# Optimization experiments

Measured on AMD Instinct MI355X. Metric: run time of the kernel, lower is better.

## Reference

```python
import jax, jax.numpy as jnp
import numpy as np
from jax import lax

B, N, C, RED = 8, 2048, 1024, 4
GN_EPS = 1e-5


def setup_inputs() -> dict:
    key = jax.random.key(0)
    ks = jax.random.split(key, 8)
    s = lambda k, shp, sc: jax.random.normal(k, shp, jnp.float32) * sc
    return dict(
        x=jax.random.normal(ks[0], (B, N, C), jnp.float32),
        qkv_w=s(ks[1], (C, 3 * C), 0.02),
        c1=jnp.float32(0.01 ** 2),
        c2=jnp.float32(0.03 ** 2),
        conv1_w=s(ks[2], (4, 1, 3), 0.3),      # OIH
        gn_g=jnp.ones(4, jnp.float32),
        gn_b=jnp.zeros(4, jnp.float32),
        conv2_w=s(ks[3], (1, 4, 3), 0.3),      # OIH
        conv2_b=jnp.zeros(1, jnp.float32),
        ch_w1=s(ks[4], (C, C // RED), 0.02),
        ch_b1=jnp.zeros(C // RED, jnp.float32),
        ch_w2=s(ks[5], (C // RED, C), 0.02),
        ch_b2=jnp.zeros(C, jnp.float32),
        proj_w=s(ks[6], (C, C), 0.02),
        proj_b=jnp.zeros(C, jnp.float32),
    )


def _conv1d(x, w):  # x:[B,Cin,N], w:[O,I,3], pad=1
    return lax.conv_general_dilated(x, w, (1,), [(1, 1)],
                                    dimension_numbers=('NCH', 'OIH', 'NCH'))


def _ode_func(A, conv1_w, gn_g, gn_b, conv2_w, conv2_b):
    # A: [B,N] -> Conv1d(1,4) -> GroupNorm(2,4) -> ReLU -> Conv1d(4,1)
    h = _conv1d(A[:, None, :], conv1_w)                 # [B,4,N]
    b, _, n = h.shape
    hg = h.reshape(b, 2, 2, n)                          # 2 groups of 2 channels
    mu = hg.mean((2, 3), keepdims=True)
    var = hg.var((2, 3), keepdims=True)
    h = ((hg - mu) * lax.rsqrt(var + GN_EPS)).reshape(b, 4, n)
    h = jax.nn.relu(h * gn_g[None, :, None] + gn_b[None, :, None])
    y = _conv1d(h, conv2_w) + conv2_b[None, :, None]    # [B,1,N]
    return y[:, 0, :]


def reference(x, qkv_w, c1, c2, conv1_w, gn_g, gn_b, conv2_w, conv2_b,
              ch_w1, ch_b1, ch_w2, ch_b2, proj_w, proj_b):
    Bx, Nx, Cx = x.shape
    qkv = (x @ qkv_w).reshape(Bx, Nx, 3, Cx)
    q, k, v = qkv[..., 0, :], qkv[..., 1, :], qkv[..., 2, :]

    # SSIM-style per-token statistics over the channel dim
    mu_q = q.mean(-1, keepdims=True)
    mu_k = k.mean(-1, keepdims=True)
    dq, dk = q - mu_q, k - mu_k
    inv_cm1 = 1.0 / (Cx - 1)
    sigma_qk = (dq * dk).sum(-1, keepdims=True) * inv_cm1
    sigma_q2 = (dq * dq).sum(-1, keepdims=True) * inv_cm1
    sigma_k2 = (dk * dk).sum(-1, keepdims=True) * inv_cm1
    num = (2 * mu_q * mu_k + c1) * (2 * sigma_qk + c2)
    den = (mu_q ** 2 + mu_k ** 2 + c1) * (sigma_q2 + sigma_k2 + c2)
    attn_base = ((num / (den + 1e-7)) ** 2)[..., 0]     # [B,N]

    # explicit-Euler integration over t = linspace(0,1,2) -> one step, dt=1
    steps = 2
    ts = jnp.linspace(0.0, 1.0, steps)
    dts = ts[1:] - ts[:-1]

    def step(A, dt):
        return A + dt * _ode_func(A, conv1_w, gn_g, gn_b, conv2_w, conv2_b), None

    A, _ = lax.scan(step, attn_base, dts)
    final_a = jax.nn.sigmoid(A)                         # [B,N]
    weights = jax.nn.softmax(final_a, axis=1)           # softmax over tokens

    # channel gating from mean token
    m = x.mean(axis=1, keepdims=True)                   # [B,1,C]
    ch_w = jax.nn.sigmoid(jax.nn.relu(m @ ch_w1 + ch_b1) @ ch_w2 + ch_b2)

    out_low = weights[..., None] * v * ch_w             # [B,N,C]
    return out_low @ proj_w + proj_b
```

## Files before the change

### kernel.cpp

```cpp
#include <hip/hip_runtime.h>

typedef __attribute__((ext_vector_type(8))) short short8;
typedef __attribute__((ext_vector_type(4))) short short4v;
typedef __attribute__((ext_vector_type(4))) float floatx4;

__device__ __forceinline__ unsigned short f2bf(float f) {
    unsigned u = __float_as_uint(f);
    u = u + 0x7fffu + ((u >> 16) & 1u);
    return (unsigned short)(u >> 16);
}

__device__ __forceinline__ void gl_lds16(const void* g, void* l) {
    __builtin_amdgcn_global_load_lds((const __attribute__((address_space(1))) void*)g,
                                     (__attribute__((address_space(3))) void*)l, 16, 0, 0);
}

__global__ __launch_bounds__(256) void convmean_kernel(const float* __restrict__ x,
                                                       short* __restrict__ xb,
                                                       float* __restrict__ part) {
    int bid = blockIdx.x;
    int b = bid >> 6, nch = bid & 63;
    int tid = threadIdx.x;
    size_t base = ((size_t)b * 2048 + nch * 32) * 1024;
    float s0 = 0.f, s1 = 0.f, s2 = 0.f, s3 = 0.f;
    int c0 = tid * 4;
    for (int r = 0; r < 32; r++) {
        const float* rp = x + base + (size_t)r * 1024 + c0;
        float4 v = *(const float4*)rp;
        s0 += v.x; s1 += v.y; s2 += v.z; s3 += v.w;
        short4v o;
        o[0] = (short)f2bf(v.x); o[1] = (short)f2bf(v.y);
        o[2] = (short)f2bf(v.z); o[3] = (short)f2bf(v.w);
        *(short4v*)(xb + base + (size_t)r * 1024 + c0) = o;
    }
    float* pp = part + ((size_t)b * 64 + nch) * 1024 + c0;
    float4 ps; ps.x = s0; ps.y = s1; ps.z = s2; ps.w = s3;
    *(float4*)pp = ps;
}

__global__ __launch_bounds__(256) void transpose_conv_kernel(const float* __restrict__ w_qkv,
                                                             short* __restrict__ qkvT,
                                                             const float* __restrict__ w_proj,
                                                             short* __restrict__ projT) {
    __shared__ float t[64][65];
    int bx = blockIdx.x;
    const float* in; short* out; int C; bool is_qkv;
    int c0, r0 = blockIdx.y * 64;
    if (bx < 48) { in = w_qkv; out = qkvT; C = 3072; c0 = bx * 64; is_qkv = true; }
    else         { in = w_proj; out = projT; C = 1024; c0 = (bx - 48) * 64; is_qkv = false; }
    int tid = threadIdx.x;
#pragma unroll
    for (int l = 0; l < 16; l++) {
        int idx = l * 256 + tid;
        int rr = idx >> 6, cc = idx & 63;
        t[rr][cc] = in[(size_t)(r0 + rr) * C + c0 + cc];
    }
    __syncthreads();
#pragma unroll
    for (int l = 0; l < 16; l++) {
        int idx = l * 256 + tid;
        int rr = idx >> 6, cc = idx & 63;
        int ro = c0 + rr;
        int rnew = ro;
        if (is_qkv) {
            if (ro < 1024) rnew = 2 * ro;
            else if (ro < 2048) rnew = 2 * (ro - 1024) + 1;
        }
        out[(size_t)rnew * 1024 + r0 + cc] = (short)f2bf(t[cc][rr]);
    }
}

__global__ __launch_bounds__(256) void ch_kernel(const float* __restrict__ part,
                                                 const float* __restrict__ w1,
                                                 const float* __restrict__ b1,
                                                 const float* __restrict__ w2,
                                                 const float* __restrict__ b2,
                                                 float* __restrict__ ch) {
    int b = blockIdx.x >> 3, cg = blockIdx.x & 7;
    int tid = threadIdx.x;
    __shared__ float mrow[1024];
    __shared__ float hid[256];
    for (int i = tid; i < 1024; i += 256) {
        float s = 0.f;
        for (int j = 0; j < 64; j++) s += part[((size_t)b * 64 + j) * 1024 + i];
        mrow[i] = s * (1.f / 2048.f);
    }
    __syncthreads();
    {
        float s0 = 0.f, s1 = 0.f, s2 = 0.f, s3 = 0.f;
        for (int i = 0; i < 1024; i += 4) {
            s0 += mrow[i] * w1[(size_t)i * 256 + tid];
            s1 += mrow[i + 1] * w1[(size_t)(i + 1) * 256 + tid];
            s2 += mrow[i + 2] * w1[(size_t)(i + 2) * 256 + tid];
            s3 += mrow[i + 3] * w1[(size_t)(i + 3) * 256 + tid];
        }
        hid[tid] = fmaxf((s0 + s1) + (s2 + s3) + b1[tid], 0.f);
    }
    __syncthreads();
    if (tid < 128) {
        int c = cg * 128 + tid;
        float s0 = 0.f, s1 = 0.f, s2 = 0.f, s3 = 0.f;
        for (int j = 0; j < 256; j += 4) {
            s0 += hid[j] * w2[(size_t)j * 1024 + c];
            s1 += hid[j + 1] * w2[(size_t)(j + 1) * 1024 + c];
            s2 += hid[j + 2] * w2[(size_t)(j + 2) * 1024 + c];
            s3 += hid[j + 3] * w2[(size_t)(j + 3) * 1024 + c];
        }
        float s = (s0 + s1) + (s2 + s3) + b2[c];
        ch[(size_t)b * 1024 + c] = 1.f / (1.f + expf(-s));
    }
}


#define KLOOP_BODY(T)                                                                   \
    {                                                                                   \
        const short* As_ = SH + ((T) & 1) * 4096;                                       \
        const short* Bs_ = SH + 8192 + ((T) & 1) * 8192;                                \
        _Pragma("unroll")                                                               \
        for (int jj = 0; jj < 4; jj++)                                                  \
            bfr[jj] = *(const short8*)(Bs_ + (wn * 64 + jj * 16 + ar) * 32 + swq);      \
        _Pragma("unroll")                                                               \
        for (int ii = 0; ii < 4; ii++)                                                  \
            af[ii] = *(const short8*)(As_ + (wm * 64 + ii * 16 + ar) * 32 + swq);       \
        __builtin_amdgcn_s_setprio(1);                                                  \
        _Pragma("unroll")                                                               \
        for (int ii = 0; ii < 4; ii++)                                                  \
            _Pragma("unroll")                                                           \
            for (int jj = 0; jj < 4; jj++)                                              \
                acc[ii][jj] =                                                           \
                    __builtin_amdgcn_mfma_f32_16x16x32_bf16(af[ii], bfr[jj], acc[ii][jj], 0, 0, 0); \
        __builtin_amdgcn_s_setprio(0);                                                  \
    }

__global__ __launch_bounds__(512, 4) void gemm_qkv_kernel(const short* __restrict__ A,
                                                          const short* __restrict__ BT,
                                                          short* __restrict__ vbuf,
                                                          const float* __restrict__ ch,
                                                          float* __restrict__ part2)
{
    __shared__ __align__(16) short SH[2 * 4096 + 2 * 8192];
    const int tid = threadIdx.x;
    const int wave = tid >> 6, lane = tid & 63;
    const int id = blockIdx.x;
    const int xcd = id & 7, j = id >> 3;
    const int bn = j % 12;
    const int bmg = j / 12;
    const int bm = bmg * 8 + xcd;
    const int wm = wave >> 2, wn = wave & 3;
    const int ar = lane & 15, quad = lane >> 4;
    const int swq = (quad ^ ((ar >> 1) & 3)) * 8;

    const int swzk = ((lane & 3) ^ ((lane >> 3) & 3)) * 8;
    const short* Ag = A + (size_t)(bm * 128 + wave * 16 + (lane >> 2)) * 1024 + swzk;
    const short* Bg = BT + (size_t)(bn * 256 + wave * 32 + (lane >> 2)) * 1024 + swzk;
    short* ASw = SH + wave * 512;
    short* BSw = SH + 8192 + wave * 1024;

    floatx4 acc[4][4];
    floatx4 zero = {0.f, 0.f, 0.f, 0.f};
#pragma unroll
    for (int i = 0; i < 4; i++)
#pragma unroll
        for (int jj = 0; jj < 4; jj++) acc[i][jj] = zero;

    auto stage = [&](int t) {
        const int sa = (t & 1) * 4096, sb2 = (t & 1) * 8192, ko = t * 32;
        gl_lds16(Ag + ko, ASw + sa);
        gl_lds16(Bg + ko, BSw + sb2);
        gl_lds16(Bg + (size_t)16 * 1024 + ko, BSw + sb2 + 512);
    };

    short8 af[4], bfr[4];

    stage(0);
    for (int t = 0; t < 31; ++t) {
        stage(t + 1);
        asm volatile("s_waitcnt vmcnt(3)" ::: "memory");
        asm volatile("s_barrier" ::: "memory");
        KLOOP_BODY(t);
        asm volatile("s_barrier" ::: "memory");
    }
    asm volatile("s_waitcnt vmcnt(0)" ::: "memory");
    asm volatile("s_barrier" ::: "memory");
    KLOOP_BODY(31);
    __syncthreads();

    if (bn < 8) {
        float* sb = (float*)SH;
#pragma unroll
        for (int i = 0; i < 4; i++) {
            float st[4][5];
#pragma unroll
            for (int r = 0; r < 4; r++)
#pragma unroll
                for (int f = 0; f < 5; f++) st[r][f] = 0.f;
#pragma unroll
            for (int jj = 0; jj < 4; jj++) {
#pragma unroll
                for (int r = 0; r < 4; r++) {
                    float val = acc[i][jj][r];
                    float other = __shfl_xor(val, 1);
                    float q = (lane & 1) ? other : val;
                    float kv = (lane & 1) ? val : other;
                    st[r][0] += q; st[r][1] += kv;
                    st[r][2] += q * q; st[r][3] += kv * kv; st[r][4] += q * kv;
                }
            }
#pragma unroll
            for (int r = 0; r < 4; r++)
#pragma unroll
                for (int f = 0; f < 5; f++) {
                    float v = st[r][f];
                    v += __shfl_xor(v, 2);
                    v += __shfl_xor(v, 4);
                    v += __shfl_xor(v, 8);
                    st[r][f] = v;
                }
            if ((lane & 15) == 0) {
#pragma unroll
                for (int r = 0; r < 4; r++)
#pragma unroll
                    for (int f = 0; f < 5; f++)
                        sb[(size_t)(wn * 128 + wm * 64 + i * 16 + quad * 4 + r) * 5 + f] = st[r][f];
            }
        }
        __syncthreads();
        if (tid < 128) {
#pragma unroll
            for (int f = 0; f < 5; f++) {
                float s = sb[(size_t)(0 * 128 + tid) * 5 + f] + sb[(size_t)(1 * 128 + tid) * 5 + f] +
                          sb[(size_t)(2 * 128 + tid) * 5 + f] + sb[(size_t)(3 * 128 + tid) * 5 + f];
                part2[(size_t)(bn * 5 + f) * 16384 + bm * 128 + tid] = s;
            }
        }
    } else {
        const int batch = bm >> 4;
        const int vcol0 = bn * 256 - 2048 + wn * 64;
        short* pbuf = SH + wave * 1024;
        float cw[4];
#pragma unroll
        for (int jj = 0; jj < 4; jj++) cw[jj] = ch[(size_t)batch * 1024 + vcol0 + jj * 16 + ar];
#pragma unroll
        for (int i = 0; i < 4; i++) {
#pragma unroll
            for (int jj = 0; jj < 4; jj++)
#pragma unroll
                for (int r = 0; r < 4; r++)
                    pbuf[(quad * 4 + r) * 64 + jj * 16 + ar] = (short)f2bf(acc[i][jj][r] * cw[jj]);
#pragma unroll
            for (int p = 0; p < 2; p++) {
                int idx = p * 512 + lane * 8;
                short8 vv = *(const short8*)(pbuf + idx);
                int grow = bm * 128 + wm * 64 + i * 16 + (idx >> 6);
                int gcol = vcol0 + (idx & 63);
                *(short8*)(vbuf + (size_t)grow * 1024 + gcol) = vv;
            }
        }
    }
}

__global__ __launch_bounds__(256) void finalize_kernel(const float* __restrict__ part2,
                                                       const float* __restrict__ c1p,
                                                       const float* __restrict__ c2p,
                                                       float* __restrict__ attn) {
    int row = blockIdx.x * 256 + threadIdx.x;
    float s[5] = {0.f, 0.f, 0.f, 0.f, 0.f};
#pragma unroll
    for (int slot = 0; slot < 8; slot++)
#pragma unroll
        for (int f = 0; f < 5; f++)
            s[f] += part2[(size_t)((slot * 5 + f) << 14) + row];
    const float C = 1024.f, invcm1 = 1.f / 1023.f;
    float c1 = *c1p, c2 = *c2p;
    float muq = s[0] / C, muk = s[1] / C;
    float sigqk = (s[4] - C * muq * muk) * invcm1;
    float sigq2 = (s[2] - C * muq * muq) * invcm1;
    float sigk2 = (s[3] - C * muk * muk) * invcm1;
    float num = (2.f * muq * muk + c1) * (2.f * sigqk + c2);
    float den = (muq * muq + muk * muk + c1) * (sigq2 + sigk2 + c2);
    float r = num / (den + 1e-7f);
    attn[row] = r * r;
}

__device__ __forceinline__ float blk_sum(float v, float* buf) {
#pragma unroll
    for (int m = 1; m < 64; m <<= 1) v += __shfl_xor(v, m);
    int wave = threadIdx.x >> 6;
    if ((threadIdx.x & 63) == 0) buf[wave] = v;
    __syncthreads();
    float r = buf[0] + buf[1] + buf[2] + buf[3];
    __syncthreads();
    return r;
}
__device__ __forceinline__ float blk_max(float v, float* buf) {
#pragma unroll
    for (int m = 1; m < 64; m <<= 1) v = fmaxf(v, __shfl_xor(v, m));
    int wave = threadIdx.x >> 6;
    if ((threadIdx.x & 63) == 0) buf[wave] = v;
    __syncthreads();
    float r = fmaxf(fmaxf(buf[0], buf[1]), fmaxf(buf[2], buf[3]));
    __syncthreads();
    return r;
}

__global__ __launch_bounds__(256) void ode_softmax_kernel(const float* __restrict__ attn,
                                                          const float* __restrict__ w1,
                                                          const float* __restrict__ gng,
                                                          const float* __restrict__ gnb,
                                                          const float* __restrict__ w2,
                                                          const float* __restrict__ b2,
                                                          float* __restrict__ wgt) {
    int b = blockIdx.x, tid = threadIdx.x;
    __shared__ float A0[2048];
    __shared__ float H[4][2048];
    __shared__ float rbuf[4];
    for (int i = tid; i < 2048; i += 256) A0[i] = attn[(size_t)b * 2048 + i];
    __syncthreads();
    float w1l[12], w2l[12];
#pragma unroll
    for (int i = 0; i < 12; i++) { w1l[i] = w1[i]; w2l[i] = w2[i]; }
    float gg[4], gb[4];
#pragma unroll
    for (int c = 0; c < 4; c++) { gg[c] = gng[c]; gb[c] = gnb[c]; }

    float s0 = 0.f, ss0 = 0.f, s1 = 0.f, ss1 = 0.f;
    for (int i = tid; i < 2048; i += 256) {
        float le = (i > 0) ? A0[i - 1] : 0.f;
        float mi = A0[i];
        float ri = (i < 2047) ? A0[i + 1] : 0.f;
#pragma unroll
        for (int c = 0; c < 4; c++) {
            float h = w1l[c * 3] * le + w1l[c * 3 + 1] * mi + w1l[c * 3 + 2] * ri;
            H[c][i] = h;
            if (c < 2) { s0 += h; ss0 += h * h; } else { s1 += h; ss1 += h * h; }
        }
    }
    s0 = blk_sum(s0, rbuf);
    ss0 = blk_sum(ss0, rbuf);
    s1 = blk_sum(s1, rbuf);
    ss1 = blk_sum(ss1, rbuf);
    float mu0 = s0 / 4096.f, var0 = ss0 / 4096.f - mu0 * mu0;
    float mu1 = s1 / 4096.f, var1 = ss1 / 4096.f - mu1 * mu1;
    float is0 = 1.f / sqrtf(var0 + 1e-5f);
    float is1 = 1.f / sqrtf(var1 + 1e-5f);

    for (int i = tid; i < 2048; i += 256) {
#pragma unroll
        for (int c = 0; c < 4; c++) {
            float inv = (c < 2) ? is0 : is1;
            float mu = (c < 2) ? mu0 : mu1;
            float v = (H[c][i] - mu) * inv * gg[c] + gb[c];
            H[c][i] = fmaxf(v, 0.f);
        }
    }
    __syncthreads();

    float bias2 = b2[0];
    float myfa[8];
    float lmax = -1e30f;
#pragma unroll
    for (int ii = 0; ii < 8; ii++) {
        int i = tid + ii * 256;
        float y = bias2;
#pragma unroll
        for (int c = 0; c < 4; c++) {
            float le = (i > 0) ? H[c][i - 1] : 0.f;
            float mi = H[c][i];
            float ri = (i < 2047) ? H[c][i + 1] : 0.f;
            y += w2l[c * 3] * le + w2l[c * 3 + 1] * mi + w2l[c * 3 + 2] * ri;
        }
        float Av = A0[i] + y;
        float fa = 1.f / (1.f + expf(-Av));
        myfa[ii] = fa;
        lmax = fmaxf(lmax, fa);
    }
    float gmax = blk_max(lmax, rbuf);
    float lsum = 0.f;
#pragma unroll
    for (int ii = 0; ii < 8; ii++) {
        myfa[ii] = expf(myfa[ii] - gmax);
        lsum += myfa[ii];
    }
    float gsum = blk_sum(lsum, rbuf);
    float inv = 1.f / gsum;
#pragma unroll
    for (int ii = 0; ii < 8; ii++) wgt[(size_t)b * 2048 + tid + ii * 256] = myfa[ii] * inv;
}

__global__ __launch_bounds__(512, 4) void gemm_out_kernel(const short* __restrict__ vbuf,
                                                          const short* __restrict__ BT,
                                                          const float* __restrict__ wgt,
                                                          const float* __restrict__ pb,
                                                          float* __restrict__ Out)
{
    __shared__ __align__(16) short SH[2 * 4096 + 2 * 8192];
    const int tid = threadIdx.x;
    const int wave = tid >> 6, lane = tid & 63;
    const int id = blockIdx.x;
    const int xcd = id & 7, j = id >> 3;
    const int bn = j & 3;
    const int bmg = j >> 2;
    const int bm = bmg * 8 + xcd;
    const int wm = wave >> 2, wn = wave & 3;
    const int ar = lane & 15, quad = lane >> 4;
    const int swq = (quad ^ ((ar >> 1) & 3)) * 8;

    const int swzk = ((lane & 3) ^ ((lane >> 3) & 3)) * 8;
    const short* Ag = vbuf + (size_t)(bm * 128 + wave * 16 + (lane >> 2)) * 1024 + swzk;
    const short* Bg = BT + (size_t)(bn * 256 + wave * 32 + (lane >> 2)) * 1024 + swzk;
    short* ASw = SH + wave * 512;
    short* BSw = SH + 8192 + wave * 1024;

    floatx4 acc[4][4];
    floatx4 zero = {0.f, 0.f, 0.f, 0.f};
#pragma unroll
    for (int i = 0; i < 4; i++)
#pragma unroll
        for (int jj = 0; jj < 4; jj++) acc[i][jj] = zero;

    auto stage = [&](int t) {
        const int sa = (t & 1) * 4096, sb2 = (t & 1) * 8192, ko = t * 32;
        gl_lds16(Ag + ko, ASw + sa);
        gl_lds16(Bg + ko, BSw + sb2);
        gl_lds16(Bg + (size_t)16 * 1024 + ko, BSw + sb2 + 512);
    };

    short8 af[4], bfr[4];

    stage(0);
    for (int t = 0; t < 31; ++t) {
        stage(t + 1);
        asm volatile("s_waitcnt vmcnt(3)" ::: "memory");
        asm volatile("s_barrier" ::: "memory");
        KLOOP_BODY(t);
        asm volatile("s_barrier" ::: "memory");
    }
    asm volatile("s_waitcnt vmcnt(0)" ::: "memory");
    asm volatile("s_barrier" ::: "memory");
    KLOOP_BODY(31);
    __syncthreads();

    const int row0 = bm * 128 + wm * 64;
    const int col0 = bn * 256 + wn * 64;
    float* obuf = (float*)SH + wave * 1024;
#pragma unroll
    for (int i = 0; i < 4; i++) {
#pragma unroll
        for (int jj = 0; jj < 4; jj++) {
            float bias = pb[col0 + jj * 16 + ar];
#pragma unroll
            for (int r = 0; r < 4; r++) {
                int grow = row0 + i * 16 + quad * 4 + r;
                obuf[(quad * 4 + r) * 64 + jj * 16 + ar] = wgt[grow] * acc[i][jj][r] + bias;
            }
        }
#pragma unroll
        for (int p = 0; p < 4; p++) {
            int idx = p * 256 + lane * 4;
            float4 vv = *(const float4*)(obuf + idx);
            int grow = row0 + i * 16 + (idx >> 6);
            int gcol = col0 + (idx & 63);
            *(float4*)(Out + (size_t)grow * 1024 + gcol) = vv;
        }
    }
}

extern "C" void kernel_launch(void* const* d_in, const int* in_sizes, int n_in,
                              void* d_out, int out_size, void* d_ws, size_t ws_size,
                              hipStream_t stream) {
    const float* x       = (const float*)d_in[0];
    const float* qkv_w   = (const float*)d_in[1];
    const float* c1      = (const float*)d_in[2];
    const float* c2      = (const float*)d_in[3];
    const float* conv1_w = (const float*)d_in[4];
    const float* gn_g    = (const float*)d_in[5];
    const float* gn_b    = (const float*)d_in[6];
    const float* conv2_w = (const float*)d_in[7];
    const float* conv2_b = (const float*)d_in[8];
    const float* ch_w1   = (const float*)d_in[9];
    const float* ch_b1   = (const float*)d_in[10];
    const float* ch_w2   = (const float*)d_in[11];
    const float* ch_b2   = (const float*)d_in[12];
    const float* proj_w  = (const float*)d_in[13];
    const float* proj_b  = (const float*)d_in[14];
    float* out = (float*)d_out;

    size_t off = 0;
    char* base = (char*)d_ws;
    auto carve = [&](size_t bytes) -> char* {
        char* p = base + off;
        off += (bytes + 255) & ~(size_t)255;
        return p;
    };
    short* x_bf  = (short*)carve((size_t)16384 * 1024 * 2);
    short* qkvT  = (short*)carve((size_t)3072 * 1024 * 2);
    short* projT = (short*)carve((size_t)1024 * 1024 * 2);
    short* vbuf  = (short*)carve((size_t)16384 * 1024 * 2);
    float* part2 = (float*)carve((size_t)80 * 16384 * 4);
    float* attn  = (float*)carve((size_t)16384 * 4);
    float* wgt   = (float*)carve((size_t)16384 * 4);
    float* part  = (float*)carve((size_t)8 * 64 * 1024 * 4);
    float* chw   = (float*)carve((size_t)8 * 1024 * 4);

    convmean_kernel<<<512, 256, 0, stream>>>(x, x_bf, part);
    transpose_conv_kernel<<<dim3(64, 16), 256, 0, stream>>>(qkv_w, qkvT, proj_w, projT);
    ch_kernel<<<64, 256, 0, stream>>>(part, ch_w1, ch_b1, ch_w2, ch_b2, chw);
    gemm_qkv_kernel<<<1536, 512, 0, stream>>>(x_bf, qkvT, vbuf, chw, part2);
    finalize_kernel<<<64, 256, 0, stream>>>(part2, c1, c2, attn);
    ode_softmax_kernel<<<8, 256, 0, stream>>>(attn, conv1_w, gn_g, gn_b, conv2_w, conv2_b, wgt);
    gemm_out_kernel<<<512, 512, 0, stream>>>(vbuf, projT, wgt, proj_b, out);
}
```

Baseline: 405.5 us.

## Switch GEMM inner loops from 16x16x32 to 32x32x16 bf16 MFMA tiles

Both GEMM kernels now compute each wave's 64x64 tile as 2x2 blocks of 32x32 MFMA instructions instead of 4x4 blocks of 16x16. This halves the LDS fragment reads per k-step and cuts the MFMA instruction count. It also changes the LDS swizzle, the accumulator register layout, and the epilogues (SSIM statistics reduction, v scaling and output write) to match the 32x32 output mapping. The risk is bank conflicts under the new swizzle and errors in the remapped epilogue indexing.

```diff
diff --git a/kernel.cpp b/kernel.cpp
--- a/kernel.cpp
+++ b/kernel.cpp
@@ -2,7 +2,7 @@
 
 typedef __attribute__((ext_vector_type(8))) short short8;
 typedef __attribute__((ext_vector_type(4))) short short4v;
-typedef __attribute__((ext_vector_type(4))) float floatx4;
+typedef __attribute__((ext_vector_type(16))) float floatx16;
 
 __device__ __forceinline__ unsigned short f2bf(float f) {
     unsigned u = __float_as_uint(f);
@@ -116,19 +116,28 @@
     {                                                                                   \
         const short* As_ = SH + ((T) & 1) * 4096;                                       \
         const short* Bs_ = SH + 8192 + ((T) & 1) * 8192;                                \
+        short8 a_[2][2], b_[2][2];                                                      \
         _Pragma("unroll")                                                               \
-        for (int jj = 0; jj < 4; jj++)                                                  \
-            bfr[jj] = *(const short8*)(Bs_ + (wn * 64 + jj * 16 + ar) * 32 + swq);      \
+        for (int mi = 0; mi < 2; mi++)                                                  \
+            _Pragma("unroll")                                                           \
+            for (int ks = 0; ks < 2; ks++)                                              \
+                a_[mi][ks] = *(const short8*)(As_ + (wm * 64 + mi * 32 + l31) * 32 +    \
+                                              ((ks * 2 + hl) ^ (l31 & 3)) * 8);        \
         _Pragma("unroll")                                                               \
-        for (int ii = 0; ii < 4; ii++)                                                  \
-            af[ii] = *(const short8*)(As_ + (wm * 64 + ii * 16 + ar) * 32 + swq);       \
+        for (int nj = 0; nj < 2; nj++)                                                  \
+            _Pragma("unroll")                                                           \
+            for (int ks = 0; ks < 2; ks++)                                              \
+                b_[nj][ks] = *(const short8*)(Bs_ + (wn * 64 + nj * 32 + l31) * 32 +    \
+                                              ((ks * 2 + hl) ^ (l31 & 3)) * 8);        \
         __builtin_amdgcn_s_setprio(1);                                                  \
         _Pragma("unroll")                                                               \
-        for (int ii = 0; ii < 4; ii++)                                                  \
+        for (int ks = 0; ks < 2; ks++)                                                  \
             _Pragma("unroll")                                                           \
-            for (int jj = 0; jj < 4; jj++)                                              \
-                acc[ii][jj] =                                                           \
-                    __builtin_amdgcn_mfma_f32_16x16x32_bf16(af[ii], bfr[jj], acc[ii][jj], 0, 0, 0); \
+            for (int mi = 0; mi < 2; mi++)                                              \
+                _Pragma("unroll")                                                       \
+                for (int nj = 0; nj < 2; nj++)                                          \
+                    acc[mi][nj] = __builtin_amdgcn_mfma_f32_32x32x16_bf16(              \
+                        a_[mi][ks], b_[nj][ks], acc[mi][nj], 0, 0, 0);                  \
         __builtin_amdgcn_s_setprio(0);                                                  \
     }
 
@@ -147,21 +156,21 @@
     const int bmg = j / 12;
     const int bm = bmg * 8 + xcd;
     const int wm = wave >> 2, wn = wave & 3;
-    const int ar = lane & 15, quad = lane >> 4;
-    const int swq = (quad ^ ((ar >> 1) & 3)) * 8;
-
-    const int swzk = ((lane & 3) ^ ((lane >> 3) & 3)) * 8;
+    const int l31 = lane & 31, hl = lane >> 5;
+
+    const int swzk = ((lane & 3) ^ ((lane >> 2) & 3)) * 8;
     const short* Ag = A + (size_t)(bm * 128 + wave * 16 + (lane >> 2)) * 1024 + swzk;
     const short* Bg = BT + (size_t)(bn * 256 + wave * 32 + (lane >> 2)) * 1024 + swzk;
     short* ASw = SH + wave * 512;
     short* BSw = SH + 8192 + wave * 1024;
 
-    floatx4 acc[4][4];
-    floatx4 zero = {0.f, 0.f, 0.f, 0.f};
-#pragma unroll
-    for (int i = 0; i < 4; i++)
-#pragma unroll
-        for (int jj = 0; jj < 4; jj++) acc[i][jj] = zero;
+    floatx16 acc[2][2];
+#pragma unroll
+    for (int i = 0; i < 2; i++)
+#pragma unroll
+        for (int jj = 0; jj < 2; jj++)
+#pragma unroll
+            for (int r = 0; r < 16; r++) acc[i][jj][r] = 0.f;
 
     auto stage = [&](int t) {
         const int sa = (t & 1) * 4096, sb2 = (t & 1) * 8192, ko = t * 32;
@@ -169,8 +178,6 @@
         gl_lds16(Bg + ko, BSw + sb2);
         gl_lds16(Bg + (size_t)16 * 1024 + ko, BSw + sb2 + 512);
     };
-
-    short8 af[4], bfr[4];
 
     stage(0);
     for (int t = 0; t < 31; ++t) {
@@ -188,40 +195,44 @@
     if (bn < 8) {
         float* sb = (float*)SH;
 #pragma unroll
-        for (int i = 0; i < 4; i++) {
-            float st[4][5];
-#pragma unroll
-            for (int r = 0; r < 4; r++)
-#pragma unroll
-                for (int f = 0; f < 5; f++) st[r][f] = 0.f;
-#pragma unroll
-            for (int jj = 0; jj < 4; jj++) {
-#pragma unroll
-                for (int r = 0; r < 4; r++) {
-                    float val = acc[i][jj][r];
-                    float other = __shfl_xor(val, 1);
-                    float q = (lane & 1) ? other : val;
-                    float kv = (lane & 1) ? val : other;
-                    st[r][0] += q; st[r][1] += kv;
-                    st[r][2] += q * q; st[r][3] += kv * kv; st[r][4] += q * kv;
+        for (int mi = 0; mi < 2; mi++) {
+#pragma unroll
+            for (int rg = 0; rg < 4; rg++) {
+                float st[4][5];
+#pragma unroll
+                for (int r = 0; r < 4; r++)
+#pragma unroll
+                    for (int f = 0; f < 5; f++) st[r][f] = 0.f;
+#pragma unroll
+                for (int nj = 0; nj < 2; nj++) {
+#pragma unroll
+                    for (int r = 0; r < 4; r++) {
+                        float val = acc[mi][nj][rg * 4 + r];
+                        float other = __shfl_xor(val, 1);
+                        float q = (lane & 1) ? other : val;
+                        float kv = (lane & 1) ? val : other;
+                        st[r][0] += q; st[r][1] += kv;
+                        st[r][2] += q * q; st[r][3] += kv * kv; st[r][4] += q * kv;
+                    }
                 }
-            }
-#pragma unroll
-            for (int r = 0; r < 4; r++)
-#pragma unroll
-                for (int f = 0; f < 5; f++) {
-                    float v = st[r][f];
-                    v += __shfl_xor(v, 2);
-                    v += __shfl_xor(v, 4);
-                    v += __shfl_xor(v, 8);
-                    st[r][f] = v;
+#pragma unroll
+                for (int r = 0; r < 4; r++)
+#pragma unroll
+                    for (int f = 0; f < 5; f++) {
+                        float v = st[r][f];
+                        v += __shfl_xor(v, 2);
+                        v += __shfl_xor(v, 4);
+                        v += __shfl_xor(v, 8);
+                        v += __shfl_xor(v, 16);
+                        st[r][f] = v;
+                    }
+                if (l31 == 0) {
+#pragma unroll
+                    for (int r = 0; r < 4; r++)
+#pragma unroll
+                        for (int f = 0; f < 5; f++)
+                            sb[(size_t)(wn * 128 + wm * 64 + mi * 32 + rg * 8 + hl * 4 + r) * 5 + f] = st[r][f];
                 }
-            if ((lane & 15) == 0) {
-#pragma unroll
-                for (int r = 0; r < 4; r++)
-#pragma unroll
-                    for (int f = 0; f < 5; f++)
-                        sb[(size_t)(wn * 128 + wm * 64 + i * 16 + quad * 4 + r) * 5 + f] = st[r][f];
             }
         }
         __syncthreads();
@@ -237,23 +248,29 @@
         const int batch = bm >> 4;
         const int vcol0 = bn * 256 - 2048 + wn * 64;
         short* pbuf = SH + wave * 1024;
-        float cw[4];
-#pragma unroll
-        for (int jj = 0; jj < 4; jj++) cw[jj] = ch[(size_t)batch * 1024 + vcol0 + jj * 16 + ar];
-#pragma unroll
-        for (int i = 0; i < 4; i++) {
-#pragma unroll
-            for (int jj = 0; jj < 4; jj++)
-#pragma unroll
-                for (int r = 0; r < 4; r++)
-                    pbuf[(quad * 4 + r) * 64 + jj * 16 + ar] = (short)f2bf(acc[i][jj][r] * cw[jj]);
-#pragma unroll
-            for (int p = 0; p < 2; p++) {
-                int idx = p * 512 + lane * 8;
-                short8 vv = *(const short8*)(pbuf + idx);
-                int grow = bm * 128 + wm * 64 + i * 16 + (idx >> 6);
-                int gcol = vcol0 + (idx & 63);
-                *(short8*)(vbuf + (size_t)grow * 1024 + gcol) = vv;
+        float cw[2];
+#pragma unroll
+        for (int nj = 0; nj < 2; nj++) cw[nj] = ch[(size_t)batch * 1024 + vcol0 + nj * 32 + l31];
+#pragma unroll
+        for (int mi = 0; mi < 2; mi++) {
+#pragma unroll
+            for (int pass = 0; pass < 2; pass++) {
+#pragma unroll
+                for (int rr = 0; rr < 8; rr++) {
+                    int reg = pass * 8 + rr;
+                    int rowl = (rr & 3) + 8 * (rr >> 2) + 4 * hl;
+#pragma unroll
+                    for (int nj = 0; nj < 2; nj++)
+                        pbuf[rowl * 64 + nj * 32 + l31] = (short)f2bf(acc[mi][nj][reg] * cw[nj]);
+                }
+#pragma unroll
+                for (int p = 0; p < 2; p++) {
+                    int idx = p * 512 + lane * 8;
+                    short8 vv = *(const short8*)(pbuf + idx);
+                    int grow = bm * 128 + wm * 64 + mi * 32 + pass * 16 + (idx >> 6);
+                    int gcol = vcol0 + (idx & 63);
+                    *(short8*)(vbuf + (size_t)grow * 1024 + gcol) = vv;
+                }
             }
         }
     }
@@ -402,21 +419,21 @@
     const int bmg = j >> 2;
     const int bm = bmg * 8 + xcd;
     const int wm = wave >> 2, wn = wave & 3;
-    const int ar = lane & 15, quad = lane >> 4;
-    const int swq = (quad ^ ((ar >> 1) & 3)) * 8;
-
-    const int swzk = ((lane & 3) ^ ((lane >> 3) & 3)) * 8;
+    const int l31 = lane & 31, hl = lane >> 5;
+
+    const int swzk = ((lane & 3) ^ ((lane >> 2) & 3)) * 8;
     const short* Ag = vbuf + (size_t)(bm * 128 + wave * 16 + (lane >> 2)) * 1024 + swzk;
     const short* Bg = BT + (size_t)(bn * 256 + wave * 32 + (lane >> 2)) * 1024 + swzk;
     short* ASw = SH + wave * 512;
     short* BSw = SH + 8192 + wave * 1024;
 
-    floatx4 acc[4][4];
-    floatx4 zero = {0.f, 0.f, 0.f, 0.f};
-#pragma unroll
-    for (int i = 0; i < 4; i++)
-#pragma unroll
-        for (int jj = 0; jj < 4; jj++) acc[i][jj] = zero;
+    floatx16 acc[2][2];
+#pragma unroll
+    for (int i = 0; i < 2; i++)
+#pragma unroll
+        for (int jj = 0; jj < 2; jj++)
+#pragma unroll
+            for (int r = 0; r < 16; r++) acc[i][jj][r] = 0.f;
 
     auto stage = [&](int t) {
         const int sa = (t & 1) * 4096, sb2 = (t & 1) * 8192, ko = t * 32;
@@ -424,8 +441,6 @@
         gl_lds16(Bg + ko, BSw + sb2);
         gl_lds16(Bg + (size_t)16 * 1024 + ko, BSw + sb2 + 512);
     };
-
-    short8 af[4], bfr[4];
 
     stage(0);
     for (int t = 0; t < 31; ++t) {
@@ -444,23 +459,29 @@
     const int col0 = bn * 256 + wn * 64;
     float* obuf = (float*)SH + wave * 1024;
 #pragma unroll
-    for (int i = 0; i < 4; i++) {
-#pragma unroll
-        for (int jj = 0; jj < 4; jj++) {
-            float bias = pb[col0 + jj * 16 + ar];
-#pragma unroll
-            for (int r = 0; r < 4; r++) {
-                int grow = row0 + i * 16 + quad * 4 + r;
-                obuf[(quad * 4 + r) * 64 + jj * 16 + ar] = wgt[grow] * acc[i][jj][r] + bias;
+    for (int mi = 0; mi < 2; mi++) {
+#pragma unroll
+        for (int pass = 0; pass < 2; pass++) {
+#pragma unroll
+            for (int rr = 0; rr < 8; rr++) {
+                int reg = pass * 8 + rr;
+                int rowl = (rr & 3) + 8 * (rr >> 2) + 4 * hl;
+                int grow = row0 + mi * 32 + pass * 16 + rowl;
+                float wg = wgt[grow];
+#pragma unroll
+                for (int nj = 0; nj < 2; nj++) {
+                    float bias = pb[col0 + nj * 32 + l31];
+                    obuf[rowl * 64 + nj * 32 + l31] = wg * acc[mi][nj][reg] + bias;
+                }
             }
-        }
-#pragma unroll
-        for (int p = 0; p < 4; p++) {
-            int idx = p * 256 + lane * 4;
-            float4 vv = *(const float4*)(obuf + idx);
-            int grow = row0 + i * 16 + (idx >> 6);
-            int gcol = col0 + (idx & 63);
-            *(float4*)(Out + (size_t)grow * 1024 + gcol) = vv;
+#pragma unroll
+            for (int p = 0; p < 4; p++) {
+                int idx = p * 256 + lane * 4;
+                float4 vv = *(const float4*)(obuf + idx);
+                int grow = row0 + mi * 32 + pass * 16 + (idx >> 6);
+                int gcol = col0 + (idx & 63);
+                *(float4*)(Out + (size_t)grow * 1024 + gcol) = vv;
+            }
         }
     }
 }
```

After: 462.1 us. 13.9% more time.
